# Performance work log

Hardware: AMD Instinct MI355X
Metric: run time of the kernel (lower is better)

## Reference

```python
import jax, jax.numpy as jnp
import numpy as np

B, S, D = 4, 4096, 1024
H, F = 16, 256
HD = D // H  # 64


def setup_inputs() -> dict:
    key = jax.random.key(0)
    ks = jax.random.split(key, 10)
    scale = 1.0 / np.sqrt(D)
    x = jax.random.normal(ks[0], (B, S, D), dtype=jnp.float32)
    Wq = jax.random.normal(ks[1], (D, D), dtype=jnp.float32) * scale
    bq = jnp.zeros((D,), dtype=jnp.float32)
    Wk = jax.random.normal(ks[2], (D, D), dtype=jnp.float32) * scale
    bk = jnp.zeros((D,), dtype=jnp.float32)
    Wv = jax.random.normal(ks[3], (D, D), dtype=jnp.float32) * scale
    bv = jnp.zeros((D,), dtype=jnp.float32)
    Wo = jax.random.normal(ks[4], (D, D), dtype=jnp.float32) * scale
    bo = jnp.zeros((D,), dtype=jnp.float32)
    rf = jax.random.normal(ks[5], (H, HD, F), dtype=jnp.float32) / np.sqrt(F)
    return {"x": x, "Wq": Wq, "bq": bq, "Wk": Wk, "bk": bk,
            "Wv": Wv, "bv": bv, "Wo": Wo, "bo": bo, "rf": rf}


def _heads(y):
    # [B,S,D] -> [B,H,S,HD]
    return y.reshape(B, S, H, HD).transpose(0, 2, 1, 3)


def reference(x, Wq, bq, Wk, bk, Wv, bv, Wo, bo, rf):
    q = _heads(x @ Wq.T + bq)
    k = _heads(x @ Wk.T + bk)
    v = _heads(x @ Wv.T + bv)
    # positive feature maps: softplus(random projection)
    q_prime = jax.nn.softplus(jnp.einsum('bhsd,hdf->bhsf', q, rf))
    k_prime = jax.nn.softplus(jnp.einsum('bhsd,hdf->bhsf', k, rf))
    kv = jnp.einsum('bhsf,bhsd->bhfd', k_prime, v)          # [B,H,F,HD]
    k_sum = k_prime.sum(axis=2)                              # [B,H,F]
    qkv = jnp.einsum('bhsf,bhfd->bhsd', q_prime, kv)        # [B,H,S,HD]
    denom = jnp.einsum('bhsf,bhf->bhs', q_prime, k_sum) + 1e-8
    out = qkv / denom[..., None]
    out = out.transpose(0, 2, 1, 3).reshape(B, S, D)
    return out @ Wo.T + bo
```

## Files before the change

kernel.cpp:

```cpp
#include <hip/hip_runtime.h>
#include <math.h>

#define Bb 4
#define Ss 4096
#define Dd 1024
#define Hh 16
#define Ff 256
#define HDd 64
#define Mm (Bb*Ss)

typedef unsigned int u32;
typedef unsigned short u16;

typedef __attribute__((ext_vector_type(8))) short bf16x8;
typedef __attribute__((ext_vector_type(4))) float f32x4;

__device__ __forceinline__ float bflo(u32 u){ union{u32 i; float f;} c; c.i = u << 16; return c.f; }
__device__ __forceinline__ float bfhi(u32 u){ union{u32 i; float f;} c; c.i = u & 0xffff0000u; return c.f; }
__device__ __forceinline__ u16 f2b(float f){
  union{float f; u32 i;} c; c.f = f;
  u32 x = c.i;
  return (u16)((x + 0x7fffu + ((x >> 16) & 1u)) >> 16);
}
__device__ __forceinline__ float softplusf(float x){
  return fmaxf(x, 0.f) + log1pf(expf(-fabsf(x)));
}
__device__ __forceinline__ float sfast(float x){
  return fmaxf(x, 0.f) + __logf(1.f + __expf(-fabsf(x)));
}

__global__ void cvt_bf16(const float* __restrict__ in, u16* __restrict__ out, int n)
{
  int i = (blockIdx.x * 256 + threadIdx.x) * 8;
  if (i >= n) return;
  float4 a = *reinterpret_cast<const float4*>(in + i);
  float4 b = *reinterpret_cast<const float4*>(in + i + 4);
  u32 w0 = (u32)f2b(a.x) | ((u32)f2b(a.y) << 16);
  u32 w1 = (u32)f2b(a.z) | ((u32)f2b(a.w) << 16);
  u32 w2 = (u32)f2b(b.x) | ((u32)f2b(b.y) << 16);
  u32 w3 = (u32)f2b(b.z) | ((u32)f2b(b.w) << 16);
  *reinterpret_cast<uint4*>(out + i) = make_uint4(w0, w1, w2, w3);
}

__global__ void zero_f32(float* __restrict__ p, int n)
{
  int i = blockIdx.x * 256 + threadIdx.x;
  if (i < n) p[i] = 0.f;
}

template<typename OT, bool BROW>
__global__ __launch_bounds__(256, 2) void mfma_gemm_bt(
    const u16* __restrict__ A, const u16* __restrict__ W,
    const float* __restrict__ bias, OT* __restrict__ C,
    int M, int N, int K)
{
  __shared__ __align__(16) u16 As[128 * 40];
  __shared__ __align__(16) u16 Bs[128 * 40];

  const int tid = threadIdx.x;
  const int wave = tid >> 6, lane = tid & 63;
  const int quad = lane >> 4, lm = lane & 15;
  const int wm = (wave >> 1) * 64, wn = (wave & 1) * 64;
  const int m0 = blockIdx.x * 128, n0 = blockIdx.y * 128;

  f32x4 acc[4][4] = {};

  for (int k0 = 0; k0 < K; k0 += 32) {
#pragma unroll
    for (int i = 0; i < 2; i++) {
      int slot = tid + 256 * i;
      int r = slot >> 2, cg = slot & 3;
      *reinterpret_cast<uint4*>(&As[r * 40 + cg * 8]) =
          *reinterpret_cast<const uint4*>(A + (size_t)(m0 + r) * K + k0 + cg * 8);
      *reinterpret_cast<uint4*>(&Bs[r * 40 + cg * 8]) =
          *reinterpret_cast<const uint4*>(W + (size_t)(n0 + r) * K + k0 + cg * 8);
    }
    __syncthreads();

    bf16x8 af[4], bf[4];
#pragma unroll
    for (int mi = 0; mi < 4; mi++)
      af[mi] = *reinterpret_cast<const bf16x8*>(&As[(wm + mi * 16 + lm) * 40 + quad * 8]);
#pragma unroll
    for (int ni = 0; ni < 4; ni++)
      bf[ni] = *reinterpret_cast<const bf16x8*>(&Bs[(wn + ni * 16 + lm) * 40 + quad * 8]);
#pragma unroll
    for (int mi = 0; mi < 4; mi++)
#pragma unroll
      for (int ni = 0; ni < 4; ni++)
        acc[mi][ni] = __builtin_amdgcn_mfma_f32_16x16x32_bf16(af[mi], bf[ni], acc[mi][ni], 0, 0, 0);
    __syncthreads();
  }

#pragma unroll
  for (int mi = 0; mi < 4; mi++)
#pragma unroll
    for (int ni = 0; ni < 4; ni++) {
      const int n = n0 + wn + ni * 16 + lm;
      const float bvn = BROW ? 0.f : bias[n];
#pragma unroll
      for (int r = 0; r < 4; r++) {
        const int m = m0 + wm + mi * 16 + quad * 4 + r;
        const float val = acc[mi][ni][r] + (BROW ? bias[m] : bvn);
        if constexpr (sizeof(OT) == 2) ((u16*)C)[(size_t)m * N + n] = f2b(val);
        else                           ((float*)C)[(size_t)m * N + n] = val;
      }
    }
}

__global__ void rf_transpose(const float* __restrict__ rf, float* __restrict__ rft)
{
  const int h = blockIdx.x, d = blockIdx.y, f = threadIdx.x;
  rft[((size_t)h * Ff + f) * HDd + d] = rf[((size_t)(h * HDd + d)) * Ff + f];
}

#define NSPLIT 8
#define SCHUNKS (Ss / NSPLIT / 64)

__global__ __launch_bounds__(256, 2) void kv_fused(
    const u16* __restrict__ Km, const u16* __restrict__ Vt,
    const float* __restrict__ rft, float* __restrict__ kv, float* __restrict__ ksum)
{
  __shared__ __align__(16) u16 RF[Ff * 64];
  __shared__ __align__(16) u16 KS[64 * 64];
  __shared__ __align__(16) u16 VS[64 * 64];
  __shared__ __align__(16) u16 PT[4][64 * 64];

  const int bh = blockIdx.x;
  const int b = bh >> 4, h = bh & 15;
  const int s0 = blockIdx.y * (Ss / NSPLIT);
  const int tid = threadIdx.x;
  const int wave = tid >> 6, lane = tid & 63;
  const int quad = lane >> 4, lm = lane & 15;
  const int F0 = wave * 64;

  {
    const float* rh = rft + (size_t)h * Ff * HDd;
#pragma unroll
    for (int i = 0; i < 8; i++) {
      int qq = tid + 256 * i;
      int r = qq >> 3, c = qq & 7;
      const float* src = rh + r * 64 + c * 8;
      float4 a = *reinterpret_cast<const float4*>(src);
      float4 e = *reinterpret_cast<const float4*>(src + 4);
      u32 w0 = (u32)f2b(a.x) | ((u32)f2b(a.y) << 16);
      u32 w1 = (u32)f2b(a.z) | ((u32)f2b(a.w) << 16);
      u32 w2 = (u32)f2b(e.x) | ((u32)f2b(e.y) << 16);
      u32 w3 = (u32)f2b(e.z) | ((u32)f2b(e.w) << 16);
      *reinterpret_cast<uint4*>((char*)RF + r * 128 + ((c ^ (r & 7)) * 16)) =
          make_uint4(w0, w1, w2, w3);
    }
  }

  f32x4 kvacc[4][4] = {};
  float kss[4] = {0.f, 0.f, 0.f, 0.f};

  for (int ch = 0; ch < SCHUNKS; ch++) {
    const int sc0 = s0 + ch * 64;
#pragma unroll
    for (int i = 0; i < 2; i++) {
      int qq = tid + 256 * i;
      int r = qq >> 3, c = qq & 7;
      uint4 kd = *reinterpret_cast<const uint4*>(
          Km + (size_t)(b * Ss + sc0 + r) * Dd + h * 64 + c * 8);
      *reinterpret_cast<uint4*>((char*)KS + r * 128 + ((c ^ (r & 7)) * 16)) = kd;
      uint4 vd = *reinterpret_cast<const uint4*>(
          Vt + (size_t)(h * 64 + r) * Mm + b * Ss + sc0 + c * 8);
      *reinterpret_cast<uint4*>((char*)VS + r * 128 + ((c ^ (r & 7)) * 16)) = vd;
    }
    __syncthreads();

    f32x4 p[4][4] = {};
#pragma unroll
    for (int ks = 0; ks < 2; ks++) {
      bf16x8 af[4], bfr[4];
#pragma unroll
      for (int mi = 0; mi < 4; mi++) {
        int row = mi * 16 + lm;
        af[mi] = *reinterpret_cast<const bf16x8*>(
            (char*)KS + row * 128 + (((ks * 4 + quad) ^ (row & 7)) * 16));
      }
#pragma unroll
      for (int ni = 0; ni < 4; ni++) {
        int row = ni * 16 + lm;
        bfr[ni] = *reinterpret_cast<const bf16x8*>(
            (char*)RF + (F0 + row) * 128 + (((ks * 4 + quad) ^ (row & 7)) * 16));
      }
#pragma unroll
      for (int mi = 0; mi < 4; mi++)
#pragma unroll
        for (int ni = 0; ni < 4; ni++)
          p[mi][ni] = __builtin_amdgcn_mfma_f32_16x16x32_bf16(af[mi], bfr[ni], p[mi][ni], 0, 0, 0);
    }

#pragma unroll
    for (int mi = 0; mi < 4; mi++)
#pragma unroll
      for (int ni = 0; ni < 4; ni++) {
        float v0 = sfast(p[mi][ni][0]);
        float v1 = sfast(p[mi][ni][1]);
        float v2 = sfast(p[mi][ni][2]);
        float v3 = sfast(p[mi][ni][3]);
        kss[ni] += (v0 + v1) + (v2 + v3);
        u32 w0 = (u32)f2b(v0) | ((u32)f2b(v1) << 16);
        u32 w1 = (u32)f2b(v2) | ((u32)f2b(v3) << 16);
        int row = ni * 16 + lm;
        int off = (row * 128 + mi * 32 + quad * 8) ^ ((row & 7) << 4);
        *reinterpret_cast<uint2*>((char*)&PT[wave][0] + off) = make_uint2(w0, w1);
      }

#pragma unroll
    for (int ks = 0; ks < 2; ks++) {
      bf16x8 a2[4], b2[4];
#pragma unroll
      for (int mi = 0; mi < 4; mi++) {
        int row = mi * 16 + lm;
        a2[mi] = *reinterpret_cast<const bf16x8*>(
            (char*)&PT[wave][0] + row * 128 + (((ks * 4 + quad) ^ (row & 7)) * 16));
      }
#pragma unroll
      for (int ni = 0; ni < 4; ni++) {
        int row = ni * 16 + lm;
        b2[ni] = *reinterpret_cast<const bf16x8*>(
            (char*)VS + row * 128 + (((ks * 4 + quad) ^ (row & 7)) * 16));
      }
#pragma unroll
      for (int mi = 0; mi < 4; mi++)
#pragma unroll
        for (int ni = 0; ni < 4; ni++)
          kvacc[mi][ni] = __builtin_amdgcn_mfma_f32_16x16x32_bf16(a2[mi], b2[ni], kvacc[mi][ni], 0, 0, 0);
    }
    __syncthreads();
  }

  float* kvp = kv + (size_t)bh * Ff * HDd;
#pragma unroll
  for (int mi = 0; mi < 4; mi++)
#pragma unroll
    for (int ni = 0; ni < 4; ni++)
#pragma unroll
      for (int rr = 0; rr < 4; rr++) {
        int f = F0 + mi * 16 + quad * 4 + rr;
        int d = ni * 16 + lm;
        atomicAdd(kvp + (size_t)f * HDd + d, kvacc[mi][ni][rr]);
      }
#pragma unroll
  for (int ni = 0; ni < 4; ni++) {
    float v = kss[ni];
    v += __shfl_xor(v, 16, 64);
    v += __shfl_xor(v, 32, 64);
    if (quad == 0) atomicAdd(ksum + (size_t)bh * Ff + F0 + ni * 16 + lm, v);
  }
}

__global__ void kvt_cvt(const float* __restrict__ kv, u16* __restrict__ kvtb)
{
  const int bh = blockIdx.x;
  const int d = threadIdx.x & 63, fg = threadIdx.x >> 6;
  const float* src = kv + (size_t)bh * Ff * HDd + d;
  u32* dst = reinterpret_cast<u32*>(kvtb + (size_t)bh * HDd * Ff + (size_t)d * Ff + fg * 64);
#pragma unroll
  for (int j = 0; j < 32; j++) {
    float v0 = src[(size_t)(fg * 64 + 2 * j) * HDd];
    float v1 = src[(size_t)(fg * 64 + 2 * j + 1) * HDd];
    dst[j] = (u32)f2b(v0) | ((u32)f2b(v1) << 16);
  }
}

__global__ __launch_bounds__(256, 2) void attn_fused(
    const u16* __restrict__ Qm, const float* __restrict__ rft,
    const u16* __restrict__ kvtb, const float* __restrict__ ksum,
    u16* __restrict__ attnb)
{
  __shared__ __align__(16) u16 P4[4][64 * 64];
  __shared__ __align__(16) float den4[64][4];

  const int bh = blockIdx.x;
  const int b = bh >> 4, h = bh & 15;
  const int s0 = blockIdx.y * (Ss / NSPLIT);
  const int tid = threadIdx.x;
  const int wave = tid >> 6, lane = tid & 63;
  const int quad = lane >> 4, lm = lane & 15;
  const int F0 = wave * 64;

  bf16x8 bfr[4][2];
  {
    const float* rh = rft + (size_t)h * Ff * HDd;
#pragma unroll
    for (int ni = 0; ni < 4; ni++) {
      const float* rrow = rh + (size_t)(F0 + ni * 16 + lm) * HDd;
#pragma unroll
      for (int ks = 0; ks < 2; ks++) {
        float4 a = *reinterpret_cast<const float4*>(rrow + ks * 32 + quad * 8);
        float4 e = *reinterpret_cast<const float4*>(rrow + ks * 32 + quad * 8 + 4);
        union { u16 a[8]; bf16x8 v; } u;
        u.a[0] = f2b(a.x); u.a[1] = f2b(a.y); u.a[2] = f2b(a.z); u.a[3] = f2b(a.w);
        u.a[4] = f2b(e.x); u.a[5] = f2b(e.y); u.a[6] = f2b(e.z); u.a[7] = f2b(e.w);
        bfr[ni][ks] = u.v;
      }
    }
  }
  bf16x8 b2r[4][2];
  {
    const u16* kb = kvtb + (size_t)bh * HDd * Ff + (size_t)(wave * 16 + lm) * Ff;
#pragma unroll
    for (int fb = 0; fb < 4; fb++)
#pragma unroll
      for (int k2 = 0; k2 < 2; k2++)
        b2r[fb][k2] = *reinterpret_cast<const bf16x8*>(kb + fb * 64 + k2 * 32 + quad * 8);
  }
  float ksv[4];
#pragma unroll
  for (int ni = 0; ni < 4; ni++)
    ksv[ni] = ksum[(size_t)bh * Ff + F0 + ni * 16 + lm];

  for (int ch = 0; ch < SCHUNKS; ch++) {
    const int sc0 = s0 + ch * 64;

    bf16x8 af[4][2];
#pragma unroll
    for (int mi = 0; mi < 4; mi++) {
      const u16* qrow = Qm + (size_t)(b * Ss + sc0 + mi * 16 + lm) * Dd + h * 64;
#pragma unroll
      for (int ks = 0; ks < 2; ks++)
        af[mi][ks] = *reinterpret_cast<const bf16x8*>(qrow + ks * 32 + quad * 8);
    }
    f32x4 p[4][4] = {};
#pragma unroll
    for (int ks = 0; ks < 2; ks++)
#pragma unroll
      for (int mi = 0; mi < 4; mi++)
#pragma unroll
        for (int ni = 0; ni < 4; ni++)
          p[mi][ni] = __builtin_amdgcn_mfma_f32_16x16x32_bf16(af[mi][ks], bfr[ni][ks], p[mi][ni], 0, 0, 0);

#pragma unroll
    for (int mi = 0; mi < 4; mi++) {
      const int sbase = mi * 16 + quad * 4;
      float dd[4] = {0.f, 0.f, 0.f, 0.f};
#pragma unroll
      for (int ni = 0; ni < 4; ni++) {
        u16 bq[4];
#pragma unroll
        for (int r = 0; r < 4; r++) {
          float v = sfast(p[mi][ni][r]);
          bq[r] = f2b(v);
          dd[r] += bflo((u32)bq[r]) * ksv[ni];
        }
        int ob0 = __shfl_xor((int)(u32)bq[0], 1, 64);
        int ob1 = __shfl_xor((int)(u32)bq[1], 1, 64);
        int ob2 = __shfl_xor((int)(u32)bq[2], 1, 64);
        int ob3 = __shfl_xor((int)(u32)bq[3], 1, 64);
        const int odd = lm & 1;
        u32 w_a = odd ? ((u32)(u16)ob2 | ((u32)bq[2] << 16)) : ((u32)bq[0] | ((u32)(u16)ob0 << 16));
        u32 w_b = odd ? ((u32)(u16)ob3 | ((u32)bq[3] << 16)) : ((u32)bq[1] | ((u32)(u16)ob1 << 16));
        const int row_a = sbase + (odd ? 2 : 0);
        const int row_b = sbase + (odd ? 3 : 1);
        const int fpb = ni * 16 + (lm & ~1);
        const int cc = fpb >> 3;
        const int bib = (fpb & 7) * 2;
        *reinterpret_cast<u32*>((char*)&P4[wave][0] + row_a * 128 + ((cc ^ (row_a & 7)) << 4) + bib) = w_a;
        *reinterpret_cast<u32*>((char*)&P4[wave][0] + row_b * 128 + ((cc ^ (row_b & 7)) << 4) + bib) = w_b;
      }
#pragma unroll
      for (int r = 0; r < 4; r++) {
        float v = dd[r];
        v += __shfl_xor(v, 1, 64);
        v += __shfl_xor(v, 2, 64);
        v += __shfl_xor(v, 4, 64);
        v += __shfl_xor(v, 8, 64);
        if (lm == 0) den4[sbase + r][wave] = v;
      }
    }
    __syncthreads();

    f32x4 acc2[4] = {};
#pragma unroll
    for (int fb = 0; fb < 4; fb++)
#pragma unroll
      for (int k2 = 0; k2 < 2; k2++) {
        bf16x8 af2[4];
#pragma unroll
        for (int mi = 0; mi < 4; mi++) {
          int row = mi * 16 + lm;
          af2[mi] = *reinterpret_cast<const bf16x8*>(
              (char*)&P4[fb][0] + row * 128 + (((k2 * 4 + quad) ^ (row & 7)) << 4));
        }
#pragma unroll
        for (int mi = 0; mi < 4; mi++)
          acc2[mi] = __builtin_amdgcn_mfma_f32_16x16x32_bf16(af2[mi], b2r[fb][k2], acc2[mi], 0, 0, 0);
      }

#pragma unroll
    for (int mi = 0; mi < 4; mi++) {
#pragma unroll
      for (int r = 0; r < 4; r++) {
        const int s = mi * 16 + quad * 4 + r;
        float4 dv = *reinterpret_cast<const float4*>(&den4[s][0]);
        const float inv = 1.f / ((dv.x + dv.y) + (dv.z + dv.w) + 1e-8f);
        attnb[(size_t)(b * Ss + sc0 + s) * Dd + h * 64 + wave * 16 + lm] =
            f2b(acc2[mi][r] * inv);
      }
    }
    __syncthreads();
  }
}

extern "C" void kernel_launch(void* const* d_in, const int* in_sizes, int n_in,
                              void* d_out, int out_size, void* d_ws, size_t ws_size,
                              hipStream_t stream)
{
  const float* x  = (const float*)d_in[0];
  const float* Wq = (const float*)d_in[1];
  const float* bq = (const float*)d_in[2];
  const float* Wk = (const float*)d_in[3];
  const float* bk = (const float*)d_in[4];
  const float* Wv = (const float*)d_in[5];
  const float* bv = (const float*)d_in[6];
  const float* Wo = (const float*)d_in[7];
  const float* bo = (const float*)d_in[8];
  const float* rf = (const float*)d_in[9];

  char* w = (char*)d_ws;
  u16* xb = (u16*)w;        w += (size_t)Mm * Dd * 2;
  u16* q  = (u16*)w;        w += (size_t)Mm * Dd * 2;
  u16* k  = (u16*)w;        w += (size_t)Mm * Dd * 2;
  u16* vt = (u16*)w;        w += (size_t)Mm * Dd * 2;
  u16* wqb = (u16*)w;       w += (size_t)Dd * Dd * 2;
  u16* wkb = (u16*)w;       w += (size_t)Dd * Dd * 2;
  u16* wvb = (u16*)w;       w += (size_t)Dd * Dd * 2;
  u16* wob = (u16*)w;       w += (size_t)Dd * Dd * 2;
  float* kv = (float*)w;    w += (size_t)(Bb * Hh) * Ff * HDd * 4;
  float* ks = (float*)w;    w += (size_t)(Bb * Hh) * Ff * 4;
  float* rft = (float*)w;   w += (size_t)Hh * Ff * HDd * 4;
  u16* kvtb = wqb;

  cvt_bf16<<<(Mm * Dd / 8 + 255) / 256, 256, 0, stream>>>(x, xb, Mm * Dd);
  cvt_bf16<<<(Dd * Dd / 8 + 255) / 256, 256, 0, stream>>>(Wq, wqb, Dd * Dd);
  cvt_bf16<<<(Dd * Dd / 8 + 255) / 256, 256, 0, stream>>>(Wk, wkb, Dd * Dd);
  cvt_bf16<<<(Dd * Dd / 8 + 255) / 256, 256, 0, stream>>>(Wv, wvb, Dd * Dd);
  cvt_bf16<<<(Dd * Dd / 8 + 255) / 256, 256, 0, stream>>>(Wo, wob, Dd * Dd);

  const int nz = (Bb * Hh) * Ff * HDd + (Bb * Hh) * Ff;
  zero_f32<<<(nz + 255) / 256, 256, 0, stream>>>(kv, nz);
  rf_transpose<<<dim3(Hh, HDd), 256, 0, stream>>>(rf, rft);

  const dim3 gg(Mm / 128, Dd / 128);
  mfma_gemm_bt<u16, false><<<gg, 256, 0, stream>>>(xb, wqb, bq, q, Mm, Dd, Dd);
  mfma_gemm_bt<u16, false><<<gg, 256, 0, stream>>>(xb, wkb, bk, k, Mm, Dd, Dd);
  const dim3 gv(Dd / 128, Mm / 128);
  mfma_gemm_bt<u16, true><<<gv, 256, 0, stream>>>(wvb, xb, bv, vt, Dd, Mm, Dd);

  kv_fused<<<dim3(Bb * Hh, NSPLIT), 256, 0, stream>>>(k, vt, rft, kv, ks);

  kvt_cvt<<<Bb * Hh, 256, 0, stream>>>(kv, kvtb);

  attn_fused<<<dim3(Bb * Hh, NSPLIT), 256, 0, stream>>>(q, rft, kvtb, ks, xb);

  mfma_gemm_bt<float, false><<<gg, 256, 0, stream>>>(xb, wob, bo, (float*)d_out, Mm, Dd, Dd);
}
```

Baseline: 531.6 us.

## Use direct global-to-LDS loads in GEMM, packed bf16 conversion, wider attention grid

The GEMM tile loads now use the global_load_lds builtin to copy operands straight into shared memory, dropping the padded 40-element row stride for an unpadded 32-element layout. Scalar bf16 rounding is replaced with a packed two-value conversion intrinsic throughout. The attention kernel gets its own sequence split (ASPLIT=16) and a higher occupancy hint so more blocks are in flight. The unpadded LDS layout may add bank conflicts on the fragment reads, and the direct-to-LDS copy writes lanes contiguously, which may or may not match the row-major indexing the reads assume.

```diff
diff --git a/kernel.cpp b/kernel.cpp
--- a/kernel.cpp
+++ b/kernel.cpp
@@ -1,4 +1,5 @@
 #include <hip/hip_runtime.h>
+#include <hip/hip_bf16.h>
 #include <math.h>
 
 #define Bb 4
@@ -22,11 +23,18 @@
   u32 x = c.i;
   return (u16)((x + 0x7fffu + ((x >> 16) & 1u)) >> 16);
 }
-__device__ __forceinline__ float softplusf(float x){
-  return fmaxf(x, 0.f) + log1pf(expf(-fabsf(x)));
+__device__ __forceinline__ u32 pk2(float lo, float hi){
+  union { __hip_bfloat162 h; u32 u; } c;
+  c.h = __float22bfloat162_rn(make_float2(lo, hi));
+  return c.u;
 }
 __device__ __forceinline__ float sfast(float x){
   return fmaxf(x, 0.f) + __logf(1.f + __expf(-fabsf(x)));
+}
+__device__ __forceinline__ void gload_lds16(const u16* g, u16* l){
+  __builtin_amdgcn_global_load_lds(
+      (const __attribute__((address_space(1))) void*)g,
+      (__attribute__((address_space(3))) void*)l, 16, 0, 0);
 }
 
 __global__ void cvt_bf16(const float* __restrict__ in, u16* __restrict__ out, int n)
@@ -35,11 +43,8 @@
   if (i >= n) return;
   float4 a = *reinterpret_cast<const float4*>(in + i);
   float4 b = *reinterpret_cast<const float4*>(in + i + 4);
-  u32 w0 = (u32)f2b(a.x) | ((u32)f2b(a.y) << 16);
-  u32 w1 = (u32)f2b(a.z) | ((u32)f2b(a.w) << 16);
-  u32 w2 = (u32)f2b(b.x) | ((u32)f2b(b.y) << 16);
-  u32 w3 = (u32)f2b(b.z) | ((u32)f2b(b.w) << 16);
-  *reinterpret_cast<uint4*>(out + i) = make_uint4(w0, w1, w2, w3);
+  *reinterpret_cast<uint4*>(out + i) =
+      make_uint4(pk2(a.x, a.y), pk2(a.z, a.w), pk2(b.x, b.y), pk2(b.z, b.w));
 }
 
 __global__ void zero_f32(float* __restrict__ p, int n)
@@ -54,8 +59,8 @@
     const float* __restrict__ bias, OT* __restrict__ C,
     int M, int N, int K)
 {
-  __shared__ __align__(16) u16 As[128 * 40];
-  __shared__ __align__(16) u16 Bs[128 * 40];
+  __shared__ __align__(16) u16 As[128 * 32];
+  __shared__ __align__(16) u16 Bs[128 * 32];
 
   const int tid = threadIdx.x;
   const int wave = tid >> 6, lane = tid & 63;
@@ -67,23 +72,23 @@
 
   for (int k0 = 0; k0 < K; k0 += 32) {
 #pragma unroll
-    for (int i = 0; i < 2; i++) {
-      int slot = tid + 256 * i;
-      int r = slot >> 2, cg = slot & 3;
-      *reinterpret_cast<uint4*>(&As[r * 40 + cg * 8]) =
-          *reinterpret_cast<const uint4*>(A + (size_t)(m0 + r) * K + k0 + cg * 8);
-      *reinterpret_cast<uint4*>(&Bs[r * 40 + cg * 8]) =
-          *reinterpret_cast<const uint4*>(W + (size_t)(n0 + r) * K + k0 + cg * 8);
+    for (int j = 0; j < 2; j++) {
+      const int c = wave * 128 + j * 64 + lane;
+      const int r = c >> 2, cg = c & 3;
+      u16* ldsA = &As[(wave * 128 + j * 64) * 8];
+      u16* ldsB = &Bs[(wave * 128 + j * 64) * 8];
+      gload_lds16(A + (size_t)(m0 + r) * K + k0 + cg * 8, ldsA);
+      gload_lds16(W + (size_t)(n0 + r) * K + k0 + cg * 8, ldsB);
     }
     __syncthreads();
 
     bf16x8 af[4], bf[4];
 #pragma unroll
     for (int mi = 0; mi < 4; mi++)
-      af[mi] = *reinterpret_cast<const bf16x8*>(&As[(wm + mi * 16 + lm) * 40 + quad * 8]);
+      af[mi] = *reinterpret_cast<const bf16x8*>(&As[(wm + mi * 16 + lm) * 32 + quad * 8]);
 #pragma unroll
     for (int ni = 0; ni < 4; ni++)
-      bf[ni] = *reinterpret_cast<const bf16x8*>(&Bs[(wn + ni * 16 + lm) * 40 + quad * 8]);
+      bf[ni] = *reinterpret_cast<const bf16x8*>(&Bs[(wn + ni * 16 + lm) * 32 + quad * 8]);
 #pragma unroll
     for (int mi = 0; mi < 4; mi++)
 #pragma unroll
@@ -143,12 +148,8 @@
       const float* src = rh + r * 64 + c * 8;
       float4 a = *reinterpret_cast<const float4*>(src);
       float4 e = *reinterpret_cast<const float4*>(src + 4);
-      u32 w0 = (u32)f2b(a.x) | ((u32)f2b(a.y) << 16);
-      u32 w1 = (u32)f2b(a.z) | ((u32)f2b(a.w) << 16);
-      u32 w2 = (u32)f2b(e.x) | ((u32)f2b(e.y) << 16);
-      u32 w3 = (u32)f2b(e.z) | ((u32)f2b(e.w) << 16);
       *reinterpret_cast<uint4*>((char*)RF + r * 128 + ((c ^ (r & 7)) * 16)) =
-          make_uint4(w0, w1, w2, w3);
+          make_uint4(pk2(a.x, a.y), pk2(a.z, a.w), pk2(e.x, e.y), pk2(e.z, e.w));
     }
   }
 
@@ -202,11 +203,10 @@
         float v2 = sfast(p[mi][ni][2]);
         float v3 = sfast(p[mi][ni][3]);
         kss[ni] += (v0 + v1) + (v2 + v3);
-        u32 w0 = (u32)f2b(v0) | ((u32)f2b(v1) << 16);
-        u32 w1 = (u32)f2b(v2) | ((u32)f2b(v3) << 16);
         int row = ni * 16 + lm;
         int off = (row * 128 + mi * 32 + quad * 8) ^ ((row & 7) << 4);
-        *reinterpret_cast<uint2*>((char*)&PT[wave][0] + off) = make_uint2(w0, w1);
+        *reinterpret_cast<uint2*>((char*)&PT[wave][0] + off) =
+            make_uint2(pk2(v0, v1), pk2(v2, v3));
       }
 
 #pragma unroll
@@ -263,11 +263,14 @@
   for (int j = 0; j < 32; j++) {
     float v0 = src[(size_t)(fg * 64 + 2 * j) * HDd];
     float v1 = src[(size_t)(fg * 64 + 2 * j + 1) * HDd];
-    dst[j] = (u32)f2b(v0) | ((u32)f2b(v1) << 16);
-  }
-}
-
-__global__ __launch_bounds__(256, 2) void attn_fused(
+    dst[j] = pk2(v0, v1);
+  }
+}
+
+#define ASPLIT 16
+#define ACHUNKS (Ss / ASPLIT / 64)
+
+__global__ __launch_bounds__(256, 4) void attn_fused(
     const u16* __restrict__ Qm, const float* __restrict__ rft,
     const u16* __restrict__ kvtb, const float* __restrict__ ksum,
     u16* __restrict__ attnb)
@@ -277,7 +280,7 @@
 
   const int bh = blockIdx.x;
   const int b = bh >> 4, h = bh & 15;
-  const int s0 = blockIdx.y * (Ss / NSPLIT);
+  const int s0 = blockIdx.y * (Ss / ASPLIT);
   const int tid = threadIdx.x;
   const int wave = tid >> 6, lane = tid & 63;
   const int quad = lane >> 4, lm = lane & 15;
@@ -293,9 +296,9 @@
       for (int ks = 0; ks < 2; ks++) {
         float4 a = *reinterpret_cast<const float4*>(rrow + ks * 32 + quad * 8);
         float4 e = *reinterpret_cast<const float4*>(rrow + ks * 32 + quad * 8 + 4);
-        union { u16 a[8]; bf16x8 v; } u;
-        u.a[0] = f2b(a.x); u.a[1] = f2b(a.y); u.a[2] = f2b(a.z); u.a[3] = f2b(a.w);
-        u.a[4] = f2b(e.x); u.a[5] = f2b(e.y); u.a[6] = f2b(e.z); u.a[7] = f2b(e.w);
+        union { u32 w[4]; bf16x8 v; } u;
+        u.w[0] = pk2(a.x, a.y); u.w[1] = pk2(a.z, a.w);
+        u.w[2] = pk2(e.x, e.y); u.w[3] = pk2(e.z, e.w);
         bfr[ni][ks] = u.v;
       }
     }
@@ -314,7 +317,7 @@
   for (int ni = 0; ni < 4; ni++)
     ksv[ni] = ksum[(size_t)bh * Ff + F0 + ni * 16 + lm];
 
-  for (int ch = 0; ch < SCHUNKS; ch++) {
+  for (int ch = 0; ch < ACHUNKS; ch++) {
     const int sc0 = s0 + ch * 64;
 
     bf16x8 af[4][2];
@@ -340,20 +343,19 @@
       float dd[4] = {0.f, 0.f, 0.f, 0.f};
 #pragma unroll
       for (int ni = 0; ni < 4; ni++) {
-        u16 bq[4];
-#pragma unroll
-        for (int r = 0; r < 4; r++) {
-          float v = sfast(p[mi][ni][r]);
-          bq[r] = f2b(v);
-          dd[r] += bflo((u32)bq[r]) * ksv[ni];
-        }
-        int ob0 = __shfl_xor((int)(u32)bq[0], 1, 64);
-        int ob1 = __shfl_xor((int)(u32)bq[1], 1, 64);
-        int ob2 = __shfl_xor((int)(u32)bq[2], 1, 64);
-        int ob3 = __shfl_xor((int)(u32)bq[3], 1, 64);
+        u32 pk01 = pk2(sfast(p[mi][ni][0]), sfast(p[mi][ni][1]));
+        u32 pk23 = pk2(sfast(p[mi][ni][2]), sfast(p[mi][ni][3]));
+        dd[0] += bflo(pk01) * ksv[ni];
+        dd[1] += bfhi(pk01) * ksv[ni];
+        dd[2] += bflo(pk23) * ksv[ni];
+        dd[3] += bfhi(pk23) * ksv[ni];
+        u32 ob01 = (u32)__shfl_xor((int)pk01, 1, 64);
+        u32 ob23 = (u32)__shfl_xor((int)pk23, 1, 64);
         const int odd = lm & 1;
-        u32 w_a = odd ? ((u32)(u16)ob2 | ((u32)bq[2] << 16)) : ((u32)bq[0] | ((u32)(u16)ob0 << 16));
-        u32 w_b = odd ? ((u32)(u16)ob3 | ((u32)bq[3] << 16)) : ((u32)bq[1] | ((u32)(u16)ob1 << 16));
+        u32 w_a = odd ? ((ob23 & 0xffffu) | (pk23 << 16))
+                      : ((pk01 & 0xffffu) | (ob01 << 16));
+        u32 w_b = odd ? ((ob23 >> 16)     | (pk23 & 0xffff0000u))
+                      : ((pk01 >> 16)     | (ob01 & 0xffff0000u));
         const int row_a = sbase + (odd ? 2 : 0);
         const int row_b = sbase + (odd ? 3 : 1);
         const int fpb = ni * 16 + (lm & ~1);
@@ -455,7 +457,7 @@
 
   kvt_cvt<<<Bb * Hh, 256, 0, stream>>>(kv, kvtb);
 
-  attn_fused<<<dim3(Bb * Hh, NSPLIT), 256, 0, stream>>>(q, rft, kvtb, ks, xb);
+  attn_fused<<<dim3(Bb * Hh, ASPLIT), 256, 0, stream>>>(q, rft, kvtb, ks, xb);
 
   mfma_gemm_bt<float, false><<<gg, 256, 0, stream>>>(xb, wob, bo, (float*)d_out, Mm, Dd, Dd);
 }
```

Result: slower. 575.3 us (+8.2%).
